# Kernel tuning notes

Measured on AMD Instinct MI355X. Metric: run time of the kernel, lower is better.

The kernel has to match this reference:

```python
import jax, jax.numpy as jnp
import numpy as np

D = 128          # embed_dim
NB = 30          # hardcoded neighbor count in neighbor_encoder
STEPS = 4        # process_steps
NSYM = 200000    # num_symbols (pad idx = NSYM)
B = 4096         # query batch
FEW = 5          # support pairs


def setup_inputs() -> dict:
    key = jax.random.key(0)
    ks = jax.random.split(key, 32)
    g = lambda i, shape, s=0.02: jax.random.normal(ks[i], shape, dtype=jnp.float32) * s
    inp = {}
    # embedding tables (row NSYM is padding, zeros)
    inp['emb'] = g(0, (NSYM + 1, D), 0.1).at[NSYM].set(0.0)
    inp['emb_var'] = g(1, (NSYM + 1, D), 0.1).at[NSYM].set(0.0)
    # neighbor attention (mean path)
    inp['nW'], inp['nWb'] = g(2, (D, 2 * D)), jnp.zeros((D,), jnp.float32)
    inp['nu'], inp['nub'] = g(3, (1, D)), jnp.zeros((1,), jnp.float32)
    # neighbor attention (var path)
    inp['nvW'], inp['nvWb'] = g(4, (D, 2 * D)), jnp.zeros((D,), jnp.float32)
    inp['nvu'], inp['nvub'] = g(5, (1, D)), jnp.zeros((1,), jnp.float32)
    # SupportEncoder: d_model=2D, d_inner=4D
    inp['p1W'], inp['p1b'] = g(6, (4 * D, 2 * D)), jnp.zeros((4 * D,), jnp.float32)
    inp['p2W'], inp['p2b'] = g(7, (2 * D, 4 * D)), jnp.zeros((2 * D,), jnp.float32)
    inp['ln_a'], inp['ln_b'] = jnp.ones((2 * D,), jnp.float32), jnp.zeros((2 * D,), jnp.float32)
    # QueryEncoder LSTMCell: input 2D, hidden 4D (torch gate order i,f,g,o)
    inp['Wih'], inp['Whh'] = g(8, (16 * D, 2 * D)), g(9, (16 * D, 4 * D))
    inp['bih'], inp['bhh'] = jnp.zeros((16 * D,), jnp.float32), jnp.zeros((16 * D,), jnp.float32)
    # connections: (..., 0)=relation idx, (..., 1)=entity idx
    inp['q_left'] = jax.random.randint(ks[10], (B, NB, 2), 0, NSYM, dtype=jnp.int32)
    inp['q_right'] = jax.random.randint(ks[11], (B, NB, 2), 0, NSYM, dtype=jnp.int32)
    inp['s_left'] = jax.random.randint(ks[12], (FEW, NB, 2), 0, NSYM, dtype=jnp.int32)
    inp['s_right'] = jax.random.randint(ks[13], (FEW, NB, 2), 0, NSYM, dtype=jnp.int32)
    return inp


def _layer_norm(z, a, b, eps=0.001):
    # faithful to torch: std with Bessel correction (ddof=1)
    mu = jnp.mean(z, axis=-1, keepdims=True)
    sigma = jnp.std(z, axis=-1, keepdims=True, ddof=1)
    return (z - mu) / (sigma + eps) * a + b


def reference(emb, emb_var, nW, nWb, nu, nub, nvW, nvWb, nvu, nvub,
              p1W, p1b, p2W, p2b, ln_a, ln_b, Wih, Whh, bih, bhh,
              q_left, q_right, s_left, s_right):

    def neighbor_encoder(conn):
        rel, ent = conn[..., 0], conn[..., 1]
        rel_e, ent_e = emb[rel], emb[ent]                      # [N, NB, D]
        cat = jnp.concatenate([rel_e, ent_e], axis=-1)         # [N, NB, 2D]
        a = jnp.tanh(cat @ nW.T + nWb) @ nu.T + nub            # [N, NB, 1]
        att = jax.nn.softmax(a[..., 0], axis=1)                # softmax over neighbors
        out = jnp.einsum('nk,nkd->nd', att, ent_e)
        rel_v, ent_v = emb_var[rel], emb_var[ent]
        catv = jnp.concatenate([rel_v, ent_v], axis=-1)
        av = jnp.tanh(catv @ nvW.T + nvWb) @ nvu.T + nvub
        attv = jax.nn.softmax(av[..., 0], axis=1)
        out_v = jnp.einsum('nk,nkd->nd', attv, ent_e)          # torch quirk: pools ent_embeds
        return jnp.tanh(out), jnp.tanh(out_v)

    def support_encoder(x):
        h = jax.nn.relu(x @ p1W.T + p1b) @ p2W.T + p2b
        return _layer_norm(h + x, ln_a, ln_b)

    def lstm_cell(x, h, c):
        gates = x @ Wih.T + bih + h @ Whh.T + bhh
        i, f, g_, o = jnp.split(gates, 4, axis=-1)
        c = jax.nn.sigmoid(f) * c + jax.nn.sigmoid(i) * jnp.tanh(g_)
        return jax.nn.sigmoid(o) * jnp.tanh(c), c

    def query_encoder(support, query):
        n = query.shape[0]
        h_r = jnp.zeros((n, 4 * D), query.dtype)
        c = jnp.zeros((n, 4 * D), query.dtype)
        h = query
        for _ in range(STEPS):
            h_r_, c = lstm_cell(query, h_r, c)
            h = query + h_r_[:, :2 * D]
            attn = jax.nn.softmax(h @ support.T, axis=1)
            r = attn @ support
            h_r = jnp.concatenate([h, r], axis=1)
        return h

    ql, qlv = neighbor_encoder(q_left)
    qr, qrv = neighbor_encoder(q_right)
    sl, slv = neighbor_encoder(s_left)
    sr, srv = neighbor_encoder(s_right)

    query = jnp.concatenate([ql, qr], axis=-1)       # [B, 2D]
    query_v = jnp.concatenate([qlv, qrv], axis=-1)
    support = jnp.concatenate([sl, sr], axis=-1)     # [FEW, 2D]
    support_v = jnp.concatenate([slv, srv], axis=-1)

    def match(q, s):
        s_g = support_encoder(s)
        q_g = support_encoder(q)
        q_f = query_encoder(s_g, q_g)
        s_mean = jnp.mean(s_g, axis=0, keepdims=True)  # [1, 2D]
        return (q_f @ s_mean.T)[:, 0]                  # [B]

    score = match(query, support)
    score_var = match(query_v, support_v)
    return jnp.stack([score, score_var])               # [2, B]
```

## Files before the change

### kernel.cpp

```cpp
#include <hip/hip_runtime.h>
#include <math.h>

#define DD    128
#define TWOD  256
#define FOURD 512
#define NBN   30
#define BQ    4096
#define FEWN  5
#define NSYM  200000
#define KTOT  768
#define NGATE 1024
#define ULIVE 256
#define TOTU  (2 * BQ + 2 * FEWN)
#define UPB   4

typedef short bf16x8 __attribute__((ext_vector_type(8)));
typedef float f32x4 __attribute__((ext_vector_type(4)));

__device__ __forceinline__ float sigmoidf_(float x) { return 1.0f / (1.0f + expf(-x)); }

__device__ __forceinline__ float ftanh(float x) {
    float e = __expf(2.0f * x);
    return 1.0f - 2.0f / (e + 1.0f);
}

__device__ __forceinline__ unsigned short f2bf(float f) {
    unsigned int u = __float_as_uint(f);
    unsigned int r = (u + 0x7fffu + ((u >> 16) & 1u)) >> 16;
    return (unsigned short)r;
}

__device__ __forceinline__ bf16x8 pack8(float4 a, float4 b) {
    union { bf16x8 v; unsigned int u[4]; } r;
    r.u[0] = ((__float_as_uint(a.x) + 0x8000u) >> 16) | ((__float_as_uint(a.y) + 0x8000u) & 0xffff0000u);
    r.u[1] = ((__float_as_uint(a.z) + 0x8000u) >> 16) | ((__float_as_uint(a.w) + 0x8000u) & 0xffff0000u);
    r.u[2] = ((__float_as_uint(b.x) + 0x8000u) >> 16) | ((__float_as_uint(b.y) + 0x8000u) & 0xffff0000u);
    r.u[3] = ((__float_as_uint(b.z) + 0x8000u) >> 16) | ((__float_as_uint(b.w) + 0x8000u) & 0xffff0000u);
    return r.v;
}

__device__ __forceinline__ void gload_lds16(const void* g, void* l) {
    __builtin_amdgcn_global_load_lds((const __attribute__((address_space(1))) unsigned int*)g,
                                     (__attribute__((address_space(3))) unsigned int*)l,
                                     16, 0, 0);
}

__global__ __launch_bounds__(256) void k_prep(
    const float* __restrict__ Wih, const float* __restrict__ Whh,
    const float* __restrict__ bih, const float* __restrict__ bhh,
    const float* __restrict__ p1W, const float* __restrict__ p2W,
    const float* __restrict__ nW, const float* __restrict__ nvW,
    unsigned short* __restrict__ Wbf, float* __restrict__ biasR,
    float* __restrict__ p1WT, float* __restrict__ p2WT,
    unsigned short* __restrict__ Nbf)
{
    int idx = blockIdx.x * 256 + threadIdx.x;
    int stride = gridDim.x * 256;
    for (int i = idx; i < NGATE * KTOT; i += stride) {
        int n = i / KTOT, k = i - n * KTOT;
        int blk = n >> 6, rem = n & 63;
        int g = rem >> 4, ul = rem & 15;
        int u = blk * 16 + ul;
        int srcrow = g * 512 + u;
        float v = (k < TWOD) ? Wih[srcrow * TWOD + k] : Whh[srcrow * FOURD + (k - TWOD)];
        Wbf[i] = f2bf(v);
    }
    for (int n = idx; n < NGATE; n += stride) {
        int blk = n >> 6, rem = n & 63;
        int g = rem >> 4, ul = rem & 15;
        int u = blk * 16 + ul;
        int srcrow = g * 512 + u;
        biasR[n] = bih[srcrow] + bhh[srcrow];
    }
    for (int i = idx; i < FOURD * TWOD; i += stride) {
        int o = i / TWOD, j = i % TWOD;
        p1WT[j * FOURD + o] = p1W[o * TWOD + j];
    }
    for (int i = idx; i < TWOD * FOURD; i += stride) {
        int o = i / FOURD, j = i % FOURD;
        p2WT[j * TWOD + o] = p2W[o * FOURD + j];
    }
    for (int i = idx; i < 2 * DD * TWOD; i += stride) {
        float v = (i < DD * TWOD) ? nW[i] : nvW[i - DD * TWOD];
        Nbf[i] = f2bf(v);
    }
}

__global__ __launch_bounds__(256, 2) void k_neighbor_v5(
    const float* __restrict__ emb, const float* __restrict__ emb_var,
    const unsigned short* __restrict__ Nbf,
    const float* __restrict__ nWb, const float* __restrict__ nu,
    const float* __restrict__ nvWb, const float* __restrict__ nvu,
    const int* __restrict__ q_left, const int* __restrict__ q_right,
    const int* __restrict__ s_left, const int* __restrict__ s_right,
    float* __restrict__ query, float* __restrict__ support)
{
    const int tid  = threadIdx.x;
    const int wave = tid >> 6, lane = tid & 63;
    const int quad = lane >> 4, m15 = lane & 15;
    const int pw   = wave >> 1;
    const int wn   = wave & 1;
    const int u0   = blockIdx.x * UPB;

    __shared__ __align__(16) float Sgf[4 * 32 * DD];
    __shared__ int   sidxL[UPB][64];
    __shared__ float aP[2][2][32];
    __shared__ float attL[2][32];

    {
        int un = tid >> 6, i = tid & 63;
        int uu_ = u0 + un; if (uu_ >= TOTU) uu_ = TOTU - 1;
        const int* conn;
        if (uu_ < BQ)                 conn = q_left  + uu_ * (NBN * 2);
        else if (uu_ < 2 * BQ)        conn = q_right + (uu_ - BQ) * (NBN * 2);
        else if (uu_ < 2 * BQ + FEWN) conn = s_left  + (uu_ - 2 * BQ) * (NBN * 2);
        else                          conn = s_right + (uu_ - 2 * BQ - FEWN) * (NBN * 2);
        sidxL[un][i] = (i < NBN * 2) ? conn[i] : NSYM;
    }

    const unsigned short* Bw = Nbf + (size_t)pw * DD * TWOD;
    const float* Wb = pw ? nvWb : nWb;
    const float* uu = pw ? nvu  : nu;
    bf16x8 Bf[4][8];
    float nb[4], un_[4];
#pragma unroll
    for (int t = 0; t < 4; ++t) {
        int n = wn * 64 + t * 16 + m15;
#pragma unroll
        for (int kt = 0; kt < 8; ++kt)
            Bf[t][kt] = *(const bf16x8*)(Bw + n * TWOD + kt * 32 + quad * 8);
        nb[t] = Wb[n];
        un_[t] = uu[n];
    }
    __syncthreads();

    for (int r = 0; r < UPB; ++r) {
        const int uidx = u0 + r;

        {
            const int g = wave;
            const float* table = (g < 2) ? emb : emb_var;
            const int side = g & 1;
            const int rl = lane >> 5;
            const int cb = lane & 31;
#pragma unroll
            for (int i = 0; i < 16; ++i) {
                const int row = 2 * i + rl;
                const int sym = sidxL[r][2 * row + side];
                const float* src = table + (size_t)sym * DD + ((cb ^ (row & 7)) << 2);
                gload_lds16(src, &Sgf[(g * 32 + 2 * i) * DD]);
            }
        }
        __syncthreads();

        const int pg = pw ? 2 : 0;
        f32x4 acc[2][4] = {};
#pragma unroll
        for (int kt = 0; kt < 8; ++kt) {
            const int g = (kt < 4) ? pg : pg + 1;
            const int cb0 = (kt & 3) * 8 + quad * 2;
            bf16x8 fa[2];
#pragma unroll
            for (int mt = 0; mt < 2; ++mt) {
                const int row = mt * 16 + m15;
                const float* rp = &Sgf[(g * 32 + row) * DD];
                const int s = row & 7;
                float4 x0 = *(const float4*)(rp + ((cb0 ^ s) << 2));
                float4 x1 = *(const float4*)(rp + (((cb0 + 1) ^ s) << 2));
                fa[mt] = pack8(x0, x1);
            }
#pragma unroll
            for (int mt = 0; mt < 2; ++mt)
#pragma unroll
                for (int nt = 0; nt < 4; ++nt)
                    acc[mt][nt] = __builtin_amdgcn_mfma_f32_16x16x32_bf16(fa[mt], Bf[nt][kt], acc[mt][nt], 0, 0, 0);
        }

        {
            float part[2][4];
#pragma unroll
            for (int mt = 0; mt < 2; ++mt)
#pragma unroll
                for (int rr = 0; rr < 4; ++rr) {
                    float s = 0.f;
#pragma unroll
                    for (int nt = 0; nt < 4; ++nt)
                        s += un_[nt] * ftanh(acc[mt][nt][rr] + nb[nt]);
                    part[mt][rr] = s;
                }
#pragma unroll
            for (int off = 1; off < 16; off <<= 1)
#pragma unroll
                for (int mt = 0; mt < 2; ++mt)
#pragma unroll
                    for (int rr = 0; rr < 4; ++rr)
                        part[mt][rr] += __shfl_xor(part[mt][rr], off, 64);
            if (m15 == 0) {
#pragma unroll
                for (int mt = 0; mt < 2; ++mt)
#pragma unroll
                    for (int rr = 0; rr < 4; ++rr)
                        aP[pw][wn][mt * 16 + quad * 4 + rr] = part[mt][rr];
            }
        }
        __syncthreads();

        if ((wave & 1) == 0 && lane < 32) {
            const int p = wave >> 1;
            float sc = (lane < NBN) ? aP[p][0][lane] + aP[p][1][lane] : -1e30f;
            float mx = sc;
#pragma unroll
            for (int off = 1; off < 32; off <<= 1) mx = fmaxf(mx, __shfl_xor(mx, off, 64));
            float e = (lane < NBN) ? __expf(sc - mx) : 0.f;
            float sum = e;
#pragma unroll
            for (int off = 1; off < 32; off <<= 1) sum += __shfl_xor(sum, off, 64);
            attL[p][lane] = e / sum;
        }
        __syncthreads();

        {
            const int p = tid >> 7;
            const int d = tid & 127;
            const int cbp = d >> 2, ofs = d & 3;
            float pool = 0.f;
#pragma unroll
            for (int k = 0; k < NBN; ++k)
                pool += attL[p][k] * Sgf[(32 + k) * DD + ((cbp ^ (k & 7)) << 2) + ofs];
            if (uidx < TOTU) {
                float* dst;
                if (uidx < BQ)                 dst = query   + ((size_t)p * BQ + uidx) * TWOD;
                else if (uidx < 2 * BQ)        dst = query   + ((size_t)p * BQ + (uidx - BQ)) * TWOD + DD;
                else if (uidx < 2 * BQ + FEWN) dst = support + ((size_t)p * FEWN + (uidx - 2 * BQ)) * TWOD;
                else                           dst = support + ((size_t)p * FEWN + (uidx - 2 * BQ - FEWN)) * TWOD + DD;
                dst[d] = ftanh(pool);
            }
        }
        __syncthreads();
    }
}

template <int RPB>
__global__ __launch_bounds__(256) void k_supenc(
    const float* __restrict__ xin, float* __restrict__ xout,
    unsigned short* __restrict__ abf,
    const float* __restrict__ p1WT, const float* __restrict__ p1b,
    const float* __restrict__ p2WT, const float* __restrict__ p2b,
    const float* __restrict__ ln_a, const float* __restrict__ ln_b)
{
    const int tid = threadIdx.x;
    const int r0 = blockIdx.x * RPB;
    __shared__ float X[RPB][TWOD];
    __shared__ float H1[RPB][FOURD];
    __shared__ float red[4][RPB][2];
    __shared__ float muv[RPB], sgv[RPB];

    for (int idx = tid; idx < RPB * TWOD; idx += 256) {
        int r = idx >> 8, j = idx & 255;
        X[r][j] = xin[(size_t)(r0 + r) * TWOD + j];
    }
    __syncthreads();

    {
        float acc[RPB][2] = {};
        for (int j = 0; j < TWOD; j += 4) {
            float w0[4], w1[4];
#pragma unroll
            for (int jj = 0; jj < 4; ++jj) {
                w0[jj] = p1WT[(j + jj) * FOURD + tid];
                w1[jj] = p1WT[(j + jj) * FOURD + tid + 256];
            }
#pragma unroll
            for (int r = 0; r < RPB; ++r) {
                float x[4] __attribute__((aligned(16)));
                *(float4*)x = *(const float4*)&X[r][j];
#pragma unroll
                for (int jj = 0; jj < 4; ++jj) {
                    acc[r][0] += x[jj] * w0[jj];
                    acc[r][1] += x[jj] * w1[jj];
                }
            }
        }
        float b0 = p1b[tid], b1 = p1b[tid + 256];
#pragma unroll
        for (int r = 0; r < RPB; ++r) {
            H1[r][tid]       = fmaxf(acc[r][0] + b0, 0.f);
            H1[r][tid + 256] = fmaxf(acc[r][1] + b1, 0.f);
        }
    }
    __syncthreads();

    float z[RPB];
    {
        float acc[RPB] = {};
        for (int j = 0; j < FOURD; j += 4) {
            float w[4];
#pragma unroll
            for (int jj = 0; jj < 4; ++jj) w[jj] = p2WT[(j + jj) * TWOD + tid];
#pragma unroll
            for (int r = 0; r < RPB; ++r) {
                float h[4] __attribute__((aligned(16)));
                *(float4*)h = *(const float4*)&H1[r][j];
#pragma unroll
                for (int jj = 0; jj < 4; ++jj) acc[r] += h[jj] * w[jj];
            }
        }
        float b = p2b[tid];
#pragma unroll
        for (int r = 0; r < RPB; ++r) z[r] = acc[r] + b + X[r][tid];
    }
    {
        float s[RPB], ss[RPB];
#pragma unroll
        for (int r = 0; r < RPB; ++r) { s[r] = z[r]; ss[r] = z[r] * z[r]; }
#pragma unroll
        for (int off = 1; off < 64; off <<= 1)
#pragma unroll
            for (int r = 0; r < RPB; ++r) {
                s[r]  += __shfl_xor(s[r],  off, 64);
                ss[r] += __shfl_xor(ss[r], off, 64);
            }
        const int wv = tid >> 6, lane = tid & 63;
        if (lane == 0) {
#pragma unroll
            for (int r = 0; r < RPB; ++r) { red[wv][r][0] = s[r]; red[wv][r][1] = ss[r]; }
        }
        __syncthreads();
        if (tid < RPB) {
            float st  = red[0][tid][0] + red[1][tid][0] + red[2][tid][0] + red[3][tid][0];
            float sst = red[0][tid][1] + red[1][tid][1] + red[2][tid][1] + red[3][tid][1];
            float mu  = st / (float)TWOD;
            float var = fmaxf((sst - (float)TWOD * mu * mu) / ((float)TWOD - 1.f), 0.f);
            muv[tid] = mu; sgv[tid] = sqrtf(var);
        }
        __syncthreads();
    }
#pragma unroll
    for (int r = 0; r < RPB; ++r) {
        float o = (z[r] - muv[r]) / (sgv[r] + 1e-3f) * ln_a[tid] + ln_b[tid];
        xout[(size_t)(r0 + r) * TWOD + tid] = o;
        if (abf) abf[(size_t)(r0 + r) * KTOT + tid] = f2bf(o);
    }
}

__global__ __launch_bounds__(256) void k_lstm_mfma(
    const unsigned short* __restrict__ Abf,
    const unsigned short* __restrict__ Wbf,
    const float* __restrict__ biasR,
    float* __restrict__ cst, float* __restrict__ hbuf,
    const int nkt)
{
    __shared__ __align__(16) unsigned short As[128 * 32];
    __shared__ __align__(16) unsigned short Bs[128 * 32];
    const int tid  = threadIdx.x;
    const int wave = tid >> 6, lane = tid & 63;
    const int quad = lane >> 4, m15 = lane & 15;
    const int m0 = blockIdx.x * 128;
    const int n0 = blockIdx.y * 128;
    const int wm = wave >> 1, wn = wave & 1;
    const int lrow = lane >> 2, lslot = lane & 3;

    f32x4 acc[4][4] = {};

    for (int kt = 0; kt < nkt; ++kt) {
        const int k0 = kt * 32;
        __syncthreads();
#pragma unroll
        for (int t = 0; t < 2; ++t) {
            int c = wave * 2 + t;
            int row = c * 16 + lrow;
            int kg = lslot ^ ((row >> 1) & 3);
            gload_lds16(Abf + (size_t)(m0 + row) * KTOT + k0 + kg * 8, As + c * 512);
            gload_lds16(Wbf + (size_t)(n0 + row) * KTOT + k0 + kg * 8, Bs + c * 512);
        }
        __syncthreads();

        bf16x8 fa[4], fb[4];
#pragma unroll
        for (int mi = 0; mi < 4; ++mi) {
            int ra = wm * 64 + mi * 16 + m15;
            int sa = quad ^ ((ra >> 1) & 3);
            fa[mi] = *(const bf16x8*)(As + ra * 32 + sa * 8);
            int rb = wn * 64 + mi * 16 + m15;
            int sb = quad ^ ((rb >> 1) & 3);
            fb[mi] = *(const bf16x8*)(Bs + rb * 32 + sb * 8);
        }
#pragma unroll
        for (int mi = 0; mi < 4; ++mi)
#pragma unroll
            for (int ni = 0; ni < 4; ++ni)
                acc[mi][ni] = __builtin_amdgcn_mfma_f32_16x16x32_bf16(fa[mi], fb[ni], acc[mi][ni], 0, 0, 0);
    }

    const int u = ((n0 + wn * 64) >> 2) + m15;
    float bg[4];
#pragma unroll
    for (int g = 0; g < 4; ++g) bg[g] = biasR[n0 + wn * 64 + g * 16 + m15];
#pragma unroll
    for (int mi = 0; mi < 4; ++mi) {
#pragma unroll
        for (int r = 0; r < 4; ++r) {
            int gm = m0 + wm * 64 + mi * 16 + quad * 4 + r;
            size_t cidx = (size_t)gm * ULIVE + u;
            float pi = acc[mi][0][r] + bg[0];
            float pf = acc[mi][1][r] + bg[1];
            float pg = acc[mi][2][r] + bg[2];
            float po = acc[mi][3][r] + bg[3];
            float cn = sigmoidf_(pf) * cst[cidx] + sigmoidf_(pi) * tanhf(pg);
            cst[cidx]  = cn;
            hbuf[cidx] = sigmoidf_(po) * tanhf(cn);
        }
    }
}

__global__ __launch_bounds__(256) void k_lstm_attn(
    const float* __restrict__ qg, const float* __restrict__ hbuf,
    const float* __restrict__ sg, unsigned short* __restrict__ Abf,
    float* __restrict__ hfin)
{
    const int tid = threadIdx.x;
    const int p   = blockIdx.y;
    const int wv = tid >> 6, lane = tid & 63;
    __shared__ float sgl[FEWN][TWOD];
    for (int idx = tid; idx < FEWN * TWOD; idx += 256)
        sgl[idx >> 8][idx & 255] = sg[p * FEWN * TWOD + idx];
    __syncthreads();
    const int j0 = lane * 4;
    for (int rr = 0; rr < 8; ++rr) {
        int row = blockIdx.x * 32 + wv * 8 + rr;
        size_t g = (size_t)p * BQ + row;
        float4 q4 = *(const float4*)(qg + g * TWOD + j0);
        float4 t4 = *(const float4*)(hbuf + g * ULIVE + j0);
        float h[4] __attribute__((aligned(16))) = {q4.x + t4.x, q4.y + t4.y, q4.z + t4.z, q4.w + t4.w};
        float sv[FEWN][4] __attribute__((aligned(16)));
        float pa[FEWN];
#pragma unroll
        for (int f = 0; f < FEWN; ++f) {
            *(float4*)sv[f] = *(const float4*)&sgl[f][j0];
            pa[f] = h[0] * sv[f][0] + h[1] * sv[f][1] + h[2] * sv[f][2] + h[3] * sv[f][3];
        }
#pragma unroll
        for (int off = 1; off < 64; off <<= 1)
#pragma unroll
            for (int f = 0; f < FEWN; ++f) pa[f] += __shfl_xor(pa[f], off, 64);
        float mx = pa[0];
#pragma unroll
        for (int f = 1; f < FEWN; ++f) mx = fmaxf(mx, pa[f]);
        float sum = 0.f, e[FEWN];
#pragma unroll
        for (int f = 0; f < FEWN; ++f) { e[f] = expf(pa[f] - mx); sum += e[f]; }
        float inv = 1.f / sum;
        float r4[4] __attribute__((aligned(16))) = {0.f, 0.f, 0.f, 0.f};
#pragma unroll
        for (int f = 0; f < FEWN; ++f) {
            float a = e[f] * inv;
#pragma unroll
            for (int q = 0; q < 4; ++q) r4[q] += a * sv[f][q];
        }
        unsigned short tb[4] __attribute__((aligned(8)));
#pragma unroll
        for (int q = 0; q < 4; ++q) tb[q] = f2bf(h[q]);
        *(uint2*)(Abf + g * KTOT + TWOD + j0) = *(uint2*)tb;
#pragma unroll
        for (int q = 0; q < 4; ++q) tb[q] = f2bf(r4[q]);
        *(uint2*)(Abf + g * KTOT + FOURD + j0) = *(uint2*)tb;
        *(float4*)(hfin + g * TWOD + j0) = *(float4*)h;
    }
}

__global__ __launch_bounds__(256) void k_score(
    const float* __restrict__ hfin, const float* __restrict__ sg, float* __restrict__ out)
{
    const int tid = threadIdx.x;
    const int p   = blockIdx.y;
    __shared__ float sm[TWOD];
    if (tid < TWOD) {
        const float* s = sg + p * FEWN * TWOD + tid;
        sm[tid] = (s[0] + s[TWOD] + s[2 * TWOD] + s[3 * TWOD] + s[4 * TWOD]) / 5.0f;
    }
    __syncthreads();
    const int wv = tid >> 6, lane = tid & 63;
    const int j0 = lane * 4;
    for (int rr = 0; rr < 8; ++rr) {
        int row = blockIdx.x * 32 + wv * 8 + rr;
        const float* h = hfin + ((size_t)p * BQ + row) * TWOD + j0;
        float4 h4 = *(const float4*)h;
        float4 s4 = *(const float4*)&sm[j0];
        float pv = h4.x * s4.x + h4.y * s4.y + h4.z * s4.z + h4.w * s4.w;
#pragma unroll
        for (int off = 1; off < 64; off <<= 1) pv += __shfl_xor(pv, off, 64);
        if (lane == 0) out[p * BQ + row] = pv;
    }
}

extern "C" void kernel_launch(void* const* d_in, const int* in_sizes, int n_in,
                              void* d_out, int out_size, void* d_ws, size_t ws_size,
                              hipStream_t stream)
{
    const float* emb     = (const float*)d_in[0];
    const float* emb_var = (const float*)d_in[1];
    const float* nW      = (const float*)d_in[2];
    const float* nWb     = (const float*)d_in[3];
    const float* nu      = (const float*)d_in[4];
    const float* nub     = (const float*)d_in[5];
    const float* nvW     = (const float*)d_in[6];
    const float* nvWb    = (const float*)d_in[7];
    const float* nvu     = (const float*)d_in[8];
    const float* nvub    = (const float*)d_in[9];
    const float* p1W     = (const float*)d_in[10];
    const float* p1b     = (const float*)d_in[11];
    const float* p2W     = (const float*)d_in[12];
    const float* p2b     = (const float*)d_in[13];
    const float* ln_a    = (const float*)d_in[14];
    const float* ln_b    = (const float*)d_in[15];
    const float* Wih     = (const float*)d_in[16];
    const float* Whh     = (const float*)d_in[17];
    const float* bih     = (const float*)d_in[18];
    const float* bhh     = (const float*)d_in[19];
    const int* q_left    = (const int*)d_in[20];
    const int* q_right   = (const int*)d_in[21];
    const int* s_left    = (const int*)d_in[22];
    const int* s_right   = (const int*)d_in[23];

    float* ws = (float*)d_ws;
    size_t o = 0;
    float* p1WT     = ws + o; o += FOURD * TWOD;
    float* p2WT     = ws + o; o += FOURD * TWOD;
    float* biasR    = ws + o; o += NGATE;
    float* query    = ws + o; o += (size_t)2 * BQ * TWOD;
    float* supportB = ws + o; o += 2 * FEWN * TWOD;
    float* qg       = ws + o; o += (size_t)2 * BQ * TWOD;
    float* sg       = ws + o; o += 2 * FEWN * TWOD;
    float* cst      = ws + o; o += (size_t)2 * BQ * ULIVE;
    float* hbuf     = ws + o; o += (size_t)2 * BQ * ULIVE;
    unsigned short* Wbf = (unsigned short*)(ws + o); o += (size_t)NGATE * KTOT / 2;
    unsigned short* Abf = (unsigned short*)(ws + o); o += (size_t)2 * BQ * KTOT / 2;
    unsigned short* Nbf = (unsigned short*)(ws + o); o += (size_t)2 * DD * TWOD / 2;
    float* hfin     = query;

    hipMemsetAsync(cst, 0, (size_t)2 * BQ * ULIVE * sizeof(float), stream);

    k_prep<<<dim3(1024), dim3(256), 0, stream>>>(Wih, Whh, bih, bhh, p1W, p2W, nW, nvW,
                                                 Wbf, biasR, p1WT, p2WT, Nbf);
    k_neighbor_v5<<<dim3((TOTU + UPB - 1) / UPB), dim3(256), 0, stream>>>(
        emb, emb_var, Nbf, nWb, nu, nvWb, nvu,
        q_left, q_right, s_left, s_right, query, supportB);
    k_supenc<8><<<dim3(2 * BQ / 8), dim3(256), 0, stream>>>(query, qg, Abf, p1WT, p1b, p2WT, p2b, ln_a, ln_b);
    k_supenc<1><<<dim3(2 * FEWN), dim3(256), 0, stream>>>(supportB, sg, (unsigned short*)nullptr,
                                                          p1WT, p1b, p2WT, p2b, ln_a, ln_b);
    for (int s = 0; s < 4; ++s) {
        k_lstm_mfma<<<dim3(2 * BQ / 128, NGATE / 128), dim3(256), 0, stream>>>(
            Abf, Wbf, biasR, cst, hbuf, s == 0 ? TWOD / 32 : KTOT / 32);
        k_lstm_attn<<<dim3(BQ / 32, 2), dim3(256), 0, stream>>>(qg, hbuf, sg, Abf, hfin);
    }
    k_score<<<dim3(BQ / 32, 2), dim3(256), 0, stream>>>(hfin, sg, (float*)d_out);
}
```

Measured before the change: 616.3 us.

## Prefetch next unit's neighbor embeddings during attention softmax and pooling

Restructures the neighbor-encoder kernel into a software pipeline. Once the MFMA pass for one unit finishes, the embedding gather for the next unit is issued while the current unit's tanh scoring, softmax and pooling run. Only the slot the pooling step still reads is double-buffered, which avoids a full second LDS buffer. The unpadded 30-row slots save gather work. Units per block grow from 4 to 8, raising LDS use per block and halving the number of blocks.

```diff
diff --git a/kernel.cpp b/kernel.cpp
--- a/kernel.cpp
+++ b/kernel.cpp
@@ -12,7 +12,8 @@
 #define NGATE 1024
 #define ULIVE 256
 #define TOTU  (2 * BQ + 2 * FEWN)
-#define UPB   4
+#define UPB   8
+#define GSZ   (NBN * DD)
 
 typedef short bf16x8 __attribute__((ext_vector_type(8)));
 typedef float f32x4 __attribute__((ext_vector_type(4)));
@@ -86,7 +87,27 @@
     }
 }
 
-__global__ __launch_bounds__(256, 2) void k_neighbor_v5(
+__device__ __forceinline__ void stage_unit(float* G, const int* sidx,
+                                           const float* emb, const float* emb_var,
+                                           int wave, int lane, int rn)
+{
+    int slot, side; const float* table;
+    if (wave == 0)      { slot = 0;            table = emb;     side = 0; }
+    else if (wave == 1) { slot = 3 + (rn & 1); table = emb;     side = 1; }
+    else if (wave == 2) { slot = 1;            table = emb_var; side = 0; }
+    else                { slot = 2;            table = emb_var; side = 1; }
+    const int rl = lane >> 5, cb = lane & 31;
+    float* base = G + slot * GSZ;
+#pragma unroll
+    for (int i = 0; i < 15; ++i) {
+        const int row = 2 * i + rl;
+        const int sym = sidx[2 * row + side];
+        const float* src = table + (size_t)sym * DD + ((cb ^ (row & 7)) << 2);
+        gload_lds16(src, base + 2 * i * DD);
+    }
+}
+
+__global__ __launch_bounds__(256, 2) void k_neighbor_v6(
     const float* __restrict__ emb, const float* __restrict__ emb_var,
     const unsigned short* __restrict__ Nbf,
     const float* __restrict__ nWb, const float* __restrict__ nu,
@@ -102,13 +123,13 @@
     const int wn   = wave & 1;
     const int u0   = blockIdx.x * UPB;
 
-    __shared__ __align__(16) float Sgf[4 * 32 * DD];
+    __shared__ __align__(16) float G[5 * GSZ + 2 * DD];
     __shared__ int   sidxL[UPB][64];
     __shared__ float aP[2][2][32];
     __shared__ float attL[2][32];
 
-    {
-        int un = tid >> 6, i = tid & 63;
+    for (int t = tid; t < UPB * 64; t += 256) {
+        int un = t >> 6, i = t & 63;
         int uu_ = u0 + un; if (uu_ >= TOTU) uu_ = TOTU - 1;
         const int* conn;
         if (uu_ < BQ)                 conn = q_left  + uu_ * (NBN * 2);
@@ -117,6 +138,9 @@
         else                          conn = s_right + (uu_ - 2 * BQ - FEWN) * (NBN * 2);
         sidxL[un][i] = (i < NBN * 2) ? conn[i] : NSYM;
     }
+    __syncthreads();
+
+    stage_unit(G, sidxL[0], emb, emb_var, wave, lane, 0);
 
     const unsigned short* Bw = Nbf + (size_t)pw * DD * TWOD;
     const float* Wb = pw ? nvWb : nWb;
@@ -136,34 +160,20 @@
 
     for (int r = 0; r < UPB; ++r) {
         const int uidx = u0 + r;
-
-        {
-            const int g = wave;
-            const float* table = (g < 2) ? emb : emb_var;
-            const int side = g & 1;
-            const int rl = lane >> 5;
-            const int cb = lane & 31;
-#pragma unroll
-            for (int i = 0; i < 16; ++i) {
-                const int row = 2 * i + rl;
-                const int sym = sidxL[r][2 * row + side];
-                const float* src = table + (size_t)sym * DD + ((cb ^ (row & 7)) << 2);
-                gload_lds16(src, &Sgf[(g * 32 + 2 * i) * DD]);
-            }
-        }
-        __syncthreads();
-
-        const int pg = pw ? 2 : 0;
+        const int g1c  = 3 + (r & 1);
+
+        const int slotA = pw ? 1 : 0;
+        const int slotB = pw ? 2 : g1c;
         f32x4 acc[2][4] = {};
 #pragma unroll
         for (int kt = 0; kt < 8; ++kt) {
-            const int g = (kt < 4) ? pg : pg + 1;
+            const float* sb = G + ((kt < 4) ? slotA : slotB) * GSZ;
             const int cb0 = (kt & 3) * 8 + quad * 2;
             bf16x8 fa[2];
 #pragma unroll
             for (int mt = 0; mt < 2; ++mt) {
                 const int row = mt * 16 + m15;
-                const float* rp = &Sgf[(g * 32 + row) * DD];
+                const float* rp = sb + row * DD;
                 const int s = row & 7;
                 float4 x0 = *(const float4*)(rp + ((cb0 ^ s) << 2));
                 float4 x1 = *(const float4*)(rp + (((cb0 + 1) ^ s) << 2));
@@ -175,6 +185,10 @@
                 for (int nt = 0; nt < 4; ++nt)
                     acc[mt][nt] = __builtin_amdgcn_mfma_f32_16x16x32_bf16(fa[mt], Bf[nt][kt], acc[mt][nt], 0, 0, 0);
         }
+        __syncthreads();
+
+        if (r + 1 < UPB)
+            stage_unit(G, sidxL[r + 1], emb, emb_var, wave, lane, r + 1);
 
         {
             float part[2][4];
@@ -223,10 +237,11 @@
             const int p = tid >> 7;
             const int d = tid & 127;
             const int cbp = d >> 2, ofs = d & 3;
+            const float* g1p = G + g1c * GSZ;
             float pool = 0.f;
 #pragma unroll
             for (int k = 0; k < NBN; ++k)
-                pool += attL[p][k] * Sgf[(32 + k) * DD + ((cbp ^ (k & 7)) << 2) + ofs];
+                pool += attL[p][k] * g1p[k * DD + ((cbp ^ (k & 7)) << 2) + ofs];
             if (uidx < TOTU) {
                 float* dst;
                 if (uidx < BQ)                 dst = query   + ((size_t)p * BQ + uidx) * TWOD;
@@ -542,7 +557,7 @@
 
     k_prep<<<dim3(1024), dim3(256), 0, stream>>>(Wih, Whh, bih, bhh, p1W, p2W, nW, nvW,
                                                  Wbf, biasR, p1WT, p2WT, Nbf);
-    k_neighbor_v5<<<dim3((TOTU + UPB - 1) / UPB), dim3(256), 0, stream>>>(
+    k_neighbor_v6<<<dim3((TOTU + UPB - 1) / UPB), dim3(256), 0, stream>>>(
         emb, emb_var, Nbf, nWb, nu, nvWb, nvu,
         q_left, q_right, s_left, s_right, query, supportB);
     k_supenc<8><<<dim3(2 * BQ / 8), dim3(256), 0, stream>>>(query, qg, Abf, p1WT, p1b, p2WT, p2b, ln_a, ln_b);
```

New measurement: 650.5 us. +5.6%, slower.

## Split neighbor encoder mean and var paths across a second grid dimension

Applied to the files above, without the earlier changes.

The neighbor kernel now launches one block per path, using blockIdx.y, instead of having one block process both the mean and var paths. Each block gathers only the 30 real neighbor rows for its own table, which roughly halves LDS use and raises the occupancy hint from 2 to 4 blocks per CU. The attention weights are split over 4 waves of 32 output columns, and pooling is split into two halves that are summed through LDS. The var-path block reads the pooled entity rows of `emb` straight from global memory instead of from LDS, which adds an extra gather for that path.

```diff
diff --git a/kernel.cpp b/kernel.cpp
--- a/kernel.cpp
+++ b/kernel.cpp
@@ -13,6 +13,7 @@
 #define ULIVE 256
 #define TOTU  (2 * BQ + 2 * FEWN)
 #define UPB   4
+#define GSZ   (NBN * DD)
 
 typedef short bf16x8 __attribute__((ext_vector_type(8)));
 typedef float f32x4 __attribute__((ext_vector_type(4)));
@@ -86,7 +87,7 @@
     }
 }
 
-__global__ __launch_bounds__(256, 2) void k_neighbor_v5(
+__global__ __launch_bounds__(256, 4) void k_neighbor_v7(
     const float* __restrict__ emb, const float* __restrict__ emb_var,
     const unsigned short* __restrict__ Nbf,
     const float* __restrict__ nWb, const float* __restrict__ nu,
@@ -98,14 +99,14 @@
     const int tid  = threadIdx.x;
     const int wave = tid >> 6, lane = tid & 63;
     const int quad = lane >> 4, m15 = lane & 15;
-    const int pw   = wave >> 1;
-    const int wn   = wave & 1;
+    const int path = blockIdx.y;
     const int u0   = blockIdx.x * UPB;
 
-    __shared__ __align__(16) float Sgf[4 * 32 * DD];
+    __shared__ __align__(16) float G[2 * GSZ + 2 * DD];
     __shared__ int   sidxL[UPB][64];
-    __shared__ float aP[2][2][32];
-    __shared__ float attL[2][32];
+    __shared__ float aP[4][32];
+    __shared__ float attL[32];
+    __shared__ float poolP[2][DD];
 
     {
         int un = tid >> 6, i = tid & 63;
@@ -118,14 +119,15 @@
         sidxL[un][i] = (i < NBN * 2) ? conn[i] : NSYM;
     }
 
-    const unsigned short* Bw = Nbf + (size_t)pw * DD * TWOD;
-    const float* Wb = pw ? nvWb : nWb;
-    const float* uu = pw ? nvu  : nu;
-    bf16x8 Bf[4][8];
-    float nb[4], un_[4];
-#pragma unroll
-    for (int t = 0; t < 4; ++t) {
-        int n = wn * 64 + t * 16 + m15;
+    const unsigned short* Bw = Nbf + (size_t)path * DD * TWOD;
+    const float* Wb  = path ? nvWb : nWb;
+    const float* uu  = path ? nvu  : nu;
+    const float* tbl = path ? emb_var : emb;
+    bf16x8 Bf[2][8];
+    float nb[2], un_[2];
+#pragma unroll
+    for (int t = 0; t < 2; ++t) {
+        int n = wave * 32 + t * 16 + m15;
 #pragma unroll
         for (int kt = 0; kt < 8; ++kt)
             Bf[t][kt] = *(const bf16x8*)(Bw + n * TWOD + kt * 32 + quad * 8);
@@ -138,32 +140,32 @@
         const int uidx = u0 + r;
 
         {
-            const int g = wave;
-            const float* table = (g < 2) ? emb : emb_var;
-            const int side = g & 1;
-            const int rl = lane >> 5;
-            const int cb = lane & 31;
-#pragma unroll
-            for (int i = 0; i < 16; ++i) {
-                const int row = 2 * i + rl;
-                const int sym = sidxL[r][2 * row + side];
-                const float* src = table + (size_t)sym * DD + ((cb ^ (row & 7)) << 2);
-                gload_lds16(src, &Sgf[(g * 32 + 2 * i) * DD]);
-            }
-        }
-        __syncthreads();
-
-        const int pg = pw ? 2 : 0;
-        f32x4 acc[2][4] = {};
+            const int slot = wave >> 1, half = wave & 1;
+            const int rl = lane >> 5, cb = lane & 31;
+            float* base = G + slot * GSZ;
+#pragma unroll
+            for (int i = 0; i < 8; ++i) {
+                const int pi = half * 8 + i;
+                if (pi < 15) {
+                    const int row = 2 * pi + rl;
+                    const int sym = sidxL[r][2 * row + slot];
+                    const float* src = tbl + (size_t)sym * DD + ((cb ^ (row & 7)) << 2);
+                    gload_lds16(src, base + 2 * pi * DD);
+                }
+            }
+        }
+        __syncthreads();
+
+        f32x4 acc[2][2] = {};
 #pragma unroll
         for (int kt = 0; kt < 8; ++kt) {
-            const int g = (kt < 4) ? pg : pg + 1;
+            const float* sb = G + ((kt < 4) ? 0 : GSZ);
             const int cb0 = (kt & 3) * 8 + quad * 2;
             bf16x8 fa[2];
 #pragma unroll
             for (int mt = 0; mt < 2; ++mt) {
                 const int row = mt * 16 + m15;
-                const float* rp = &Sgf[(g * 32 + row) * DD];
+                const float* rp = sb + row * DD;
                 const int s = row & 7;
                 float4 x0 = *(const float4*)(rp + ((cb0 ^ s) << 2));
                 float4 x1 = *(const float4*)(rp + (((cb0 + 1) ^ s) << 2));
@@ -172,7 +174,7 @@
 #pragma unroll
             for (int mt = 0; mt < 2; ++mt)
 #pragma unroll
-                for (int nt = 0; nt < 4; ++nt)
+                for (int nt = 0; nt < 2; ++nt)
                     acc[mt][nt] = __builtin_amdgcn_mfma_f32_16x16x32_bf16(fa[mt], Bf[nt][kt], acc[mt][nt], 0, 0, 0);
         }
 
@@ -184,7 +186,7 @@
                 for (int rr = 0; rr < 4; ++rr) {
                     float s = 0.f;
 #pragma unroll
-                    for (int nt = 0; nt < 4; ++nt)
+                    for (int nt = 0; nt < 2; ++nt)
                         s += un_[nt] * ftanh(acc[mt][nt][rr] + nb[nt]);
                     part[mt][rr] = s;
                 }
@@ -200,14 +202,14 @@
                 for (int mt = 0; mt < 2; ++mt)
 #pragma unroll
                     for (int rr = 0; rr < 4; ++rr)
-                        aP[pw][wn][mt * 16 + quad * 4 + rr] = part[mt][rr];
-            }
-        }
-        __syncthreads();
-
-        if ((wave & 1) == 0 && lane < 32) {
-            const int p = wave >> 1;
-            float sc = (lane < NBN) ? aP[p][0][lane] + aP[p][1][lane] : -1e30f;
+                        aP[wave][mt * 16 + quad * 4 + rr] = part[mt][rr];
+            }
+        }
+        __syncthreads();
+
+        if (wave == 0 && lane < 32) {
+            float sc = (lane < NBN) ? aP[0][lane] + aP[1][lane] + aP[2][lane] + aP[3][lane]
+                                    : -1e30f;
             float mx = sc;
 #pragma unroll
             for (int off = 1; off < 32; off <<= 1) mx = fmaxf(mx, __shfl_xor(mx, off, 64));
@@ -215,28 +217,41 @@
             float sum = e;
 #pragma unroll
             for (int off = 1; off < 32; off <<= 1) sum += __shfl_xor(sum, off, 64);
-            attL[p][lane] = e / sum;
+            attL[lane] = e / sum;
         }
         __syncthreads();
 
         {
-            const int p = tid >> 7;
-            const int d = tid & 127;
-            const int cbp = d >> 2, ofs = d & 3;
-            float pool = 0.f;
-#pragma unroll
-            for (int k = 0; k < NBN; ++k)
-                pool += attL[p][k] * Sgf[(32 + k) * DD + ((cbp ^ (k & 7)) << 2) + ofs];
-            if (uidx < TOTU) {
-                float* dst;
-                if (uidx < BQ)                 dst = query   + ((size_t)p * BQ + uidx) * TWOD;
-                else if (uidx < 2 * BQ)        dst = query   + ((size_t)p * BQ + (uidx - BQ)) * TWOD + DD;
-                else if (uidx < 2 * BQ + FEWN) dst = support + ((size_t)p * FEWN + (uidx - 2 * BQ)) * TWOD;
-                else                           dst = support + ((size_t)p * FEWN + (uidx - 2 * BQ - FEWN)) * TWOD + DD;
-                dst[d] = ftanh(pool);
-            }
-        }
-        __syncthreads();
+            const int half = tid >> 7, d = tid & 127;
+            const int k0 = half * 15;
+            float pp = 0.f;
+            if (path == 0) {
+                const float* g1p = G + GSZ;
+                const int cbp = d >> 2, ofs = d & 3;
+#pragma unroll
+                for (int k = k0; k < k0 + 15; ++k)
+                    pp += attL[k] * g1p[k * DD + ((cbp ^ (k & 7)) << 2) + ofs];
+            } else {
+#pragma unroll
+                for (int k = k0; k < k0 + 15; ++k) {
+                    const int sym = sidxL[r][2 * k + 1];
+                    pp += attL[k] * emb[(size_t)sym * DD + d];
+                }
+            }
+            poolP[half][d] = pp;
+        }
+        __syncthreads();
+
+        if (tid < DD && uidx < TOTU) {
+            const int d = tid;
+            float pool = poolP[0][d] + poolP[1][d];
+            float* dst;
+            if (uidx < BQ)                 dst = query   + ((size_t)path * BQ + uidx) * TWOD;
+            else if (uidx < 2 * BQ)        dst = query   + ((size_t)path * BQ + (uidx - BQ)) * TWOD + DD;
+            else if (uidx < 2 * BQ + FEWN) dst = support + ((size_t)path * FEWN + (uidx - 2 * BQ)) * TWOD;
+            else                           dst = support + ((size_t)path * FEWN + (uidx - 2 * BQ - FEWN)) * TWOD + DD;
+            dst[d] = ftanh(pool);
+        }
     }
 }
 
@@ -542,7 +557,7 @@
 
     k_prep<<<dim3(1024), dim3(256), 0, stream>>>(Wih, Whh, bih, bhh, p1W, p2W, nW, nvW,
                                                  Wbf, biasR, p1WT, p2WT, Nbf);
-    k_neighbor_v5<<<dim3((TOTU + UPB - 1) / UPB), dim3(256), 0, stream>>>(
+    k_neighbor_v7<<<dim3((TOTU + UPB - 1) / UPB, 2), dim3(256), 0, stream>>>(
         emb, emb_var, Nbf, nWb, nu, nvWb, nvu,
         q_left, q_right, s_left, s_right, query, supportB);
     k_supenc<8><<<dim3(2 * BQ / 8), dim3(256), 0, stream>>>(query, qg, Abf, p1WT, p1b, p2WT, p2b, ln_a, ln_b);
```

New measurement: 747.1 us. 1.21x slower.

## Convert embedding tables to bf16 and gather bf16 rows in neighbor kernel

Applied to the files above, without the earlier changes.

A new pre-pass kernel converts both full embedding tables from fp32 to bf16 on every call. The neighbor kernel then gathers half-size rows into LDS and feeds them to MFMA directly, with no per-tile fp32-to-bf16 packing, using an XOR swizzle suited to the new layout. The block grows to 512 threads handling 8 units: four waves per path, each covering 32 output columns, and the attention pooling is split into two halves of the neighbor range. This cuts random gather traffic and LDS usage, but it adds a full streaming read and write of both tables each call and lowers precision of the pooled embeddings.

```diff
diff --git a/kernel.cpp b/kernel.cpp
--- a/kernel.cpp
+++ b/kernel.cpp
@@ -12,7 +12,7 @@
 #define NGATE 1024
 #define ULIVE 256
 #define TOTU  (2 * BQ + 2 * FEWN)
-#define UPB   4
+#define UPB   8
 
 typedef short bf16x8 __attribute__((ext_vector_type(8)));
 typedef float f32x4 __attribute__((ext_vector_type(4)));
@@ -28,6 +28,10 @@
     unsigned int u = __float_as_uint(f);
     unsigned int r = (u + 0x7fffu + ((u >> 16) & 1u)) >> 16;
     return (unsigned short)r;
+}
+
+__device__ __forceinline__ float bf2f(unsigned short s) {
+    return __uint_as_float(((unsigned int)s) << 16);
 }
 
 __device__ __forceinline__ bf16x8 pack8(float4 a, float4 b) {
@@ -43,6 +47,23 @@
     __builtin_amdgcn_global_load_lds((const __attribute__((address_space(1))) unsigned int*)g,
                                      (__attribute__((address_space(3))) unsigned int*)l,
                                      16, 0, 0);
+}
+
+__global__ __launch_bounds__(256) void k_conv(
+    const float* __restrict__ emb, const float* __restrict__ emb_var,
+    unsigned short* __restrict__ embB, unsigned short* __restrict__ evB)
+{
+    const size_t total = (size_t)(NSYM + 1) * DD / 8;
+    size_t idx = (size_t)blockIdx.x * 256 + threadIdx.x;
+    size_t stride = (size_t)gridDim.x * 256;
+    for (size_t i = idx; i < total; i += stride) {
+        const float* s = emb + i * 8;
+        float4 a = *(const float4*)s, b = *(const float4*)(s + 4);
+        *(bf16x8*)(embB + i * 8) = pack8(a, b);
+        const float* s2 = emb_var + i * 8;
+        float4 a2 = *(const float4*)s2, b2 = *(const float4*)(s2 + 4);
+        *(bf16x8*)(evB + i * 8) = pack8(a2, b2);
+    }
 }
 
 __global__ __launch_bounds__(256) void k_prep(
@@ -86,8 +107,8 @@
     }
 }
 
-__global__ __launch_bounds__(256, 2) void k_neighbor_v5(
-    const float* __restrict__ emb, const float* __restrict__ emb_var,
+__global__ __launch_bounds__(512, 4) void k_neighbor_v8(
+    const unsigned short* __restrict__ embB, const unsigned short* __restrict__ evB,
     const unsigned short* __restrict__ Nbf,
     const float* __restrict__ nWb, const float* __restrict__ nu,
     const float* __restrict__ nvWb, const float* __restrict__ nvu,
@@ -98,14 +119,15 @@
     const int tid  = threadIdx.x;
     const int wave = tid >> 6, lane = tid & 63;
     const int quad = lane >> 4, m15 = lane & 15;
-    const int pw   = wave >> 1;
-    const int wn   = wave & 1;
+    const int path = wave >> 2;
+    const int wq   = wave & 3;
     const int u0   = blockIdx.x * UPB;
 
-    __shared__ __align__(16) float Sgf[4 * 32 * DD];
+    __shared__ __align__(16) unsigned short Gb[4 * 32 * DD];
     __shared__ int   sidxL[UPB][64];
-    __shared__ float aP[2][2][32];
+    __shared__ float aP[2][4][32];
     __shared__ float attL[2][32];
+    __shared__ float poolP[2][2][DD];
 
     {
         int un = tid >> 6, i = tid & 63;
@@ -118,14 +140,14 @@
         sidxL[un][i] = (i < NBN * 2) ? conn[i] : NSYM;
     }
 
-    const unsigned short* Bw = Nbf + (size_t)pw * DD * TWOD;
-    const float* Wb = pw ? nvWb : nWb;
-    const float* uu = pw ? nvu  : nu;
-    bf16x8 Bf[4][8];
-    float nb[4], un_[4];
-#pragma unroll
-    for (int t = 0; t < 4; ++t) {
-        int n = wn * 64 + t * 16 + m15;
+    const unsigned short* Bw = Nbf + (size_t)path * DD * TWOD;
+    const float* Wb = path ? nvWb : nWb;
+    const float* uu = path ? nvu  : nu;
+    bf16x8 Bf[2][8];
+    float nb[2], un_[2];
+#pragma unroll
+    for (int t = 0; t < 2; ++t) {
+        int n = wq * 32 + t * 16 + m15;
 #pragma unroll
         for (int kt = 0; kt < 8; ++kt)
             Bf[t][kt] = *(const bf16x8*)(Bw + n * TWOD + kt * 32 + quad * 8);
@@ -138,41 +160,37 @@
         const int uidx = u0 + r;
 
         {
-            const int g = wave;
-            const float* table = (g < 2) ? emb : emb_var;
+            const int g = wave >> 1, h = wave & 1;
+            const unsigned short* table = (g < 2) ? embB : evB;
             const int side = g & 1;
-            const int rl = lane >> 5;
-            const int cb = lane & 31;
-#pragma unroll
-            for (int i = 0; i < 16; ++i) {
-                const int row = 2 * i + rl;
+            const int rs = lane >> 4, c = lane & 15;
+#pragma unroll
+            for (int i = 0; i < 4; ++i) {
+                const int row = h * 16 + i * 4 + rs;
                 const int sym = sidxL[r][2 * row + side];
-                const float* src = table + (size_t)sym * DD + ((cb ^ (row & 7)) << 2);
-                gload_lds16(src, &Sgf[(g * 32 + 2 * i) * DD]);
-            }
-        }
-        __syncthreads();
-
-        const int pg = pw ? 2 : 0;
-        f32x4 acc[2][4] = {};
+                const unsigned short* src = table + (size_t)sym * DD + ((c ^ (row & 15)) << 3);
+                gload_lds16(src, &Gb[(g * 32 + h * 16 + i * 4) * DD]);
+            }
+        }
+        __syncthreads();
+
+        const int gA = path ? 2 : 0;
+        const int gB = path ? 3 : 1;
+        f32x4 acc[2][2] = {};
 #pragma unroll
         for (int kt = 0; kt < 8; ++kt) {
-            const int g = (kt < 4) ? pg : pg + 1;
-            const int cb0 = (kt & 3) * 8 + quad * 2;
+            const int g = (kt < 4) ? gA : gB;
             bf16x8 fa[2];
 #pragma unroll
             for (int mt = 0; mt < 2; ++mt) {
                 const int row = mt * 16 + m15;
-                const float* rp = &Sgf[(g * 32 + row) * DD];
-                const int s = row & 7;
-                float4 x0 = *(const float4*)(rp + ((cb0 ^ s) << 2));
-                float4 x1 = *(const float4*)(rp + (((cb0 + 1) ^ s) << 2));
-                fa[mt] = pack8(x0, x1);
+                const int ch = ((kt & 3) * 4 + quad) ^ (row & 15);
+                fa[mt] = *(const bf16x8*)&Gb[(g * 32 + row) * DD + ch * 8];
             }
 #pragma unroll
             for (int mt = 0; mt < 2; ++mt)
 #pragma unroll
-                for (int nt = 0; nt < 4; ++nt)
+                for (int nt = 0; nt < 2; ++nt)
                     acc[mt][nt] = __builtin_amdgcn_mfma_f32_16x16x32_bf16(fa[mt], Bf[nt][kt], acc[mt][nt], 0, 0, 0);
         }
 
@@ -184,7 +202,7 @@
                 for (int rr = 0; rr < 4; ++rr) {
                     float s = 0.f;
 #pragma unroll
-                    for (int nt = 0; nt < 4; ++nt)
+                    for (int nt = 0; nt < 2; ++nt)
                         s += un_[nt] * ftanh(acc[mt][nt][rr] + nb[nt]);
                     part[mt][rr] = s;
                 }
@@ -200,14 +218,15 @@
                 for (int mt = 0; mt < 2; ++mt)
 #pragma unroll
                     for (int rr = 0; rr < 4; ++rr)
-                        aP[pw][wn][mt * 16 + quad * 4 + rr] = part[mt][rr];
-            }
-        }
-        __syncthreads();
-
-        if ((wave & 1) == 0 && lane < 32) {
-            const int p = wave >> 1;
-            float sc = (lane < NBN) ? aP[p][0][lane] + aP[p][1][lane] : -1e30f;
+                        aP[path][wq][mt * 16 + quad * 4 + rr] = part[mt][rr];
+            }
+        }
+        __syncthreads();
+
+        if ((wave & 3) == 0 && lane < 32) {
+            const int p = path;
+            float sc = (lane < NBN) ? aP[p][0][lane] + aP[p][1][lane] + aP[p][2][lane] + aP[p][3][lane]
+                                    : -1e30f;
             float mx = sc;
 #pragma unroll
             for (int off = 1; off < 32; off <<= 1) mx = fmaxf(mx, __shfl_xor(mx, off, 64));
@@ -220,23 +239,30 @@
         __syncthreads();
 
         {
-            const int p = tid >> 7;
+            const int p = tid >> 8;
+            const int half = (tid >> 7) & 1;
             const int d = tid & 127;
-            const int cbp = d >> 2, ofs = d & 3;
-            float pool = 0.f;
-#pragma unroll
-            for (int k = 0; k < NBN; ++k)
-                pool += attL[p][k] * Sgf[(32 + k) * DD + ((cbp ^ (k & 7)) << 2) + ofs];
-            if (uidx < TOTU) {
-                float* dst;
-                if (uidx < BQ)                 dst = query   + ((size_t)p * BQ + uidx) * TWOD;
-                else if (uidx < 2 * BQ)        dst = query   + ((size_t)p * BQ + (uidx - BQ)) * TWOD + DD;
-                else if (uidx < 2 * BQ + FEWN) dst = support + ((size_t)p * FEWN + (uidx - 2 * BQ)) * TWOD;
-                else                           dst = support + ((size_t)p * FEWN + (uidx - 2 * BQ - FEWN)) * TWOD + DD;
-                dst[d] = ftanh(pool);
-            }
-        }
-        __syncthreads();
+            const int k0 = half * 15;
+            float pp = 0.f;
+#pragma unroll
+            for (int k = k0; k < k0 + 15; ++k) {
+                const int ch = (d >> 3) ^ (k & 15);
+                pp += attL[p][k] * bf2f(Gb[(32 + k) * DD + ch * 8 + (d & 7)]);
+            }
+            poolP[p][half][d] = pp;
+        }
+        __syncthreads();
+
+        if (tid < 256 && uidx < TOTU) {
+            const int p = tid >> 7, d = tid & 127;
+            float pool = poolP[p][0][d] + poolP[p][1][d];
+            float* dst;
+            if (uidx < BQ)                 dst = query   + ((size_t)p * BQ + uidx) * TWOD;
+            else if (uidx < 2 * BQ)        dst = query   + ((size_t)p * BQ + (uidx - BQ)) * TWOD + DD;
+            else if (uidx < 2 * BQ + FEWN) dst = support + ((size_t)p * FEWN + (uidx - 2 * BQ)) * TWOD;
+            else                           dst = support + ((size_t)p * FEWN + (uidx - 2 * BQ - FEWN)) * TWOD + DD;
+            dst[d] = ftanh(pool);
+        }
     }
 }
 
@@ -536,14 +562,17 @@
     unsigned short* Wbf = (unsigned short*)(ws + o); o += (size_t)NGATE * KTOT / 2;
     unsigned short* Abf = (unsigned short*)(ws + o); o += (size_t)2 * BQ * KTOT / 2;
     unsigned short* Nbf = (unsigned short*)(ws + o); o += (size_t)2 * DD * TWOD / 2;
+    unsigned short* embB = (unsigned short*)(ws + o); o += (size_t)(NSYM + 1) * DD / 2;
+    unsigned short* evB  = (unsigned short*)(ws + o); o += (size_t)(NSYM + 1) * DD / 2;
     float* hfin     = query;
 
     hipMemsetAsync(cst, 0, (size_t)2 * BQ * ULIVE * sizeof(float), stream);
 
+    k_conv<<<dim3(2048), dim3(256), 0, stream>>>(emb, emb_var, embB, evB);
     k_prep<<<dim3(1024), dim3(256), 0, stream>>>(Wih, Whh, bih, bhh, p1W, p2W, nW, nvW,
                                                  Wbf, biasR, p1WT, p2WT, Nbf);
-    k_neighbor_v5<<<dim3((TOTU + UPB - 1) / UPB), dim3(256), 0, stream>>>(
-        emb, emb_var, Nbf, nWb, nu, nvWb, nvu,
+    k_neighbor_v8<<<dim3((TOTU + UPB - 1) / UPB), dim3(512), 0, stream>>>(
+        embB, evB, Nbf, nWb, nu, nvWb, nvu,
         q_left, q_right, s_left, s_right, query, supportB);
     k_supenc<8><<<dim3(2 * BQ / 8), dim3(256), 0, stream>>>(query, qg, Abf, p1WT, p1b, p2WT, p2b, ln_a, ln_b);
     k_supenc<1><<<dim3(2 * FEWN), dim3(256), 0, stream>>>(supportB, sg, (unsigned short*)nullptr,
```

Result: slower. 734.0 us (+19.1%).
